# Kernel optimization log

Measured on AMD Instinct MI355X. Metric: run time of the kernel, lower is better.

The kernel has to match this reference:

```python
import jax, jax.numpy as jnp
import numpy as np

B, T, D, H = 2, 2048, 1024, 16
DK = D // H


def setup_inputs() -> dict:
    key = jax.random.key(0)
    ks = jax.random.split(key, 12)
    s = 1.0 / np.sqrt(D)
    inp = {
        "q_inp": jax.random.normal(ks[0], (B, T, D), jnp.float32),
        "k_inp": jax.random.normal(ks[1], (B, T, D), jnp.float32),
        "v_inp": jax.random.normal(ks[2], (B, T, D), jnp.float32),
        # causal mask: True = position is masked out
        "attn_mask": jnp.triu(jnp.ones((T, T), jnp.bool_), k=1),
        "Wq": jax.random.uniform(ks[3], (D, D), jnp.float32, -s, s),
        "bq": jax.random.uniform(ks[4], (D,), jnp.float32, -s, s),
        "Wk": jax.random.uniform(ks[5], (D, D), jnp.float32, -s, s),
        "bk": jax.random.uniform(ks[6], (D,), jnp.float32, -s, s),
        "Wv": jax.random.uniform(ks[7], (D, D), jnp.float32, -s, s),
        "bv": jax.random.uniform(ks[8], (D,), jnp.float32, -s, s),
        "Wo": jax.random.uniform(ks[9], (D, D), jnp.float32, -s, s),
        "bo": jax.random.uniform(ks[10], (D,), jnp.float32, -s, s),
    }
    return inp


def _split_heads(x):
    # [B,T,D] -> [B,H,T,DK]
    Bx, Tx, _ = x.shape
    return x.reshape(Bx, Tx, H, DK).transpose(0, 2, 1, 3)


def reference(q_inp, k_inp, v_inp, attn_mask, Wq, bq, Wk, bk, Wv, bv, Wo, bo):
    Q = _split_heads(q_inp @ Wq + bq)
    K = _split_heads(k_inp @ Wk + bk)
    V = _split_heads(v_inp @ Wv + bv)
    scale = 1.0 / jnp.sqrt(jnp.asarray(DK, Q.dtype))
    scores = jnp.einsum("bhqd,bhkd->bhqk", Q, K) * scale  # [B,H,T,T]
    scores = jnp.where(attn_mask, -jnp.inf, scores)
    attn = jax.nn.softmax(scores, axis=-1)  # dropout p=0 -> identity
    ctx = jnp.einsum("bhqk,bhkd->bhqd", attn, V)
    out = ctx.transpose(0, 2, 1, 3).reshape(B, T, D) @ Wo + bo
    return (out, attn)
```

## Files before the change

### kernel.cpp

```cpp
#include <hip/hip_runtime.h>
#include <hip/hip_bf16.h>
#include <math.h>


typedef unsigned short bfu;
typedef __attribute__((ext_vector_type(8))) short short8;
typedef __attribute__((ext_vector_type(4))) float f32x4;

#define AS1(p) ((const __attribute__((address_space(1))) void*)(p))
#define AS3(p) ((__attribute__((address_space(3))) void*)(p))
#define SOFT_C 16.0f

__device__ __forceinline__ void gld16(const void* g, void* l) {
  __builtin_amdgcn_global_load_lds(AS1(g), AS3(l), 16, 0, 0);
}

__device__ __forceinline__ bfu f2bf(float f) {
  unsigned int u = __float_as_uint(f);
  u = (u + 0x7fffu + ((u >> 16) & 1u)) >> 16;
  return (bfu)u;
}
__device__ __forceinline__ float bf2f(bfu b) {
  return __uint_as_float(((unsigned int)b) << 16);
}
__device__ __forceinline__ short8 lds_read8(const bfu* p) {
  return *reinterpret_cast<const short8*>(p);
}

__global__ __launch_bounds__(256) void cvt_x_kernel(
    const float* __restrict__ q, const float* __restrict__ k,
    const float* __restrict__ v, bfu* __restrict__ out) {
  size_t idx = ((size_t)blockIdx.x * 256 + threadIdx.x) * 8;
  const float* src; size_t off;
  if (idx < 4194304u)       { src = q; off = idx; }
  else if (idx < 8388608u)  { src = k; off = idx - 4194304u; }
  else                      { src = v; off = idx - 8388608u; }
  float4 a = *reinterpret_cast<const float4*>(src + off);
  float4 b = *reinterpret_cast<const float4*>(src + off + 4);
  short8 r;
  r[0] = (short)f2bf(a.x); r[1] = (short)f2bf(a.y);
  r[2] = (short)f2bf(a.z); r[3] = (short)f2bf(a.w);
  r[4] = (short)f2bf(b.x); r[5] = (short)f2bf(b.y);
  r[6] = (short)f2bf(b.z); r[7] = (short)f2bf(b.w);
  *reinterpret_cast<short8*>(out + idx) = r;
}

__global__ __launch_bounds__(256) void cvt_wt_kernel(
    const float* __restrict__ Wq, const float* __restrict__ Wk,
    const float* __restrict__ Wv, const float* __restrict__ Wo,
    bfu* __restrict__ Wt) {
  __shared__ float tile[32][33];
  const int z = blockIdx.z;
  const float* W = z == 0 ? Wq : z == 1 ? Wk : z == 2 ? Wv : Wo;
  bfu* out = Wt + (size_t)z * 1048576;
  const int n0 = blockIdx.x * 32, k0 = blockIdx.y * 32;
  const int tx = threadIdx.x, ty = threadIdx.y;
#pragma unroll
  for (int i = 0; i < 4; ++i)
    tile[ty + i * 8][tx] = W[(size_t)(k0 + ty + i * 8) * 1024 + n0 + tx];
  __syncthreads();
#pragma unroll
  for (int i = 0; i < 4; ++i)
    out[(size_t)(n0 + ty + i * 8) * 1024 + k0 + tx] = f2bf(tile[tx][ty + i * 8]);
}

template <int MODE>
__global__ __launch_bounds__(256) void gemm_bt_kernel(
    const bfu* __restrict__ Aall, const bfu* __restrict__ Btall,
    const float* __restrict__ bias0, const float* __restrict__ bias1,
    const float* __restrict__ bias2, bfu* __restrict__ outQKV,
    float* __restrict__ outF) {
  __shared__ bfu sA[128 * 64];
  __shared__ bfu sB[128 * 64];
  const int z = blockIdx.z;
  const int m0 = blockIdx.x * 128, n0 = blockIdx.y * 128;
  const bfu* A = Aall + (size_t)z * 4194304;
  const bfu* Bt = Btall + (size_t)z * 1048576;
  const float* bias = (z == 0) ? bias0 : (z == 1 ? bias1 : bias2);
  const int tid = threadIdx.x, w = tid >> 6, l = tid & 63;
  const int quad = l >> 4, lane16 = l & 15;
  const int l7 = lane16 & 7;
  const int mb = (w >> 1) * 64, nb = (w & 1) * 64;

  f32x4 acc[4][4] = {};

  for (int kt = 0; kt < 16; ++kt) {
    const int k0 = kt * 64;
    __syncthreads();
#pragma unroll
    for (int j = 0; j < 4; ++j) {
      const int chunk = (w * 4 + j) * 64 + l;
      const int row = chunk >> 3, c = (chunk & 7) ^ (row & 7);
      gld16(A + (size_t)(m0 + row) * 1024 + k0 + c * 8, sA + chunk * 8);
      gld16(Bt + (size_t)(n0 + row) * 1024 + k0 + c * 8, sB + chunk * 8);
    }
    __syncthreads();
#pragma unroll
    for (int ks = 0; ks < 2; ++ks) {
      const int cf = ((ks * 4 + quad) ^ l7) * 8;
      short8 af[4], bfr[4];
#pragma unroll
      for (int x = 0; x < 4; ++x) {
        af[x]  = lds_read8(sA + (mb + x * 16 + lane16) * 64 + cf);
        bfr[x] = lds_read8(sB + (nb + x * 16 + lane16) * 64 + cf);
      }
#pragma unroll
      for (int mi = 0; mi < 4; ++mi)
#pragma unroll
        for (int ni = 0; ni < 4; ++ni)
          acc[mi][ni] = __builtin_amdgcn_mfma_f32_16x16x32_bf16(
              af[mi], bfr[ni], acc[mi][ni], 0, 0, 0);
    }
  }

#pragma unroll
  for (int ni = 0; ni < 4; ++ni) {
    const int n = n0 + nb + ni * 16 + lane16;
    const float bv = bias[n];
#pragma unroll
    for (int mi = 0; mi < 4; ++mi) {
#pragma unroll
      for (int r = 0; r < 4; ++r) {
        const int m = m0 + mb + mi * 16 + quad * 4 + r;
        float v = acc[mi][ni][r] + bv;
        if (MODE == 0) {
          if (z == 0) v *= 0.125f;
          const int b = m >> 11, t = m & 2047;
          const int h = n >> 6, dk = n & 63;
          outQKV[(size_t)z * 4194304 +
                 (((size_t)(b * 16 + h) * 2048 + t) * 64 + dk)] = f2bf(v);
        } else {
          outF[(size_t)m * 1024 + n] = v;
        }
      }
    }
  }
}

__global__ __launch_bounds__(256) void vt_kernel(const bfu* __restrict__ V,
                                                 bfu* __restrict__ vT) {
  __shared__ bfu sT[64][72];
  const int bh = blockIdx.y, t0 = blockIdx.x * 64;
  const int tid = threadIdx.x;
  const bfu* src = V + (size_t)bh * 131072 + (size_t)t0 * 64;
#pragma unroll
  for (int j = 0; j < 2; ++j) {
    const int ch = j * 256 + tid;
    const int row = ch >> 3, c = ch & 7;
    short8 v = *reinterpret_cast<const short8*>(src + row * 64 + c * 8);
#pragma unroll
    for (int e = 0; e < 8; ++e) sT[c * 8 + e][row] = (bfu)v[e];
  }
  __syncthreads();
#pragma unroll
  for (int j = 0; j < 2; ++j) {
    const int ch = j * 256 + tid;
    const int d = ch >> 3, c = ch & 7;
    short8 o = lds_read8(&sT[d][c * 8]);
    *reinterpret_cast<short8*>(vT + (size_t)bh * 131072 + (size_t)d * 2048 +
                               t0 + c * 8) = o;
  }
}

__global__ __launch_bounds__(256) void attn_kernel(
    const bfu* __restrict__ qkv, const bfu* __restrict__ vT,
    float* __restrict__ attnO, bfu* __restrict__ ctx) {
  __shared__ bfu sK[2][64 * 64];
  __shared__ bfu sVt[2][64 * 64];
  __shared__ bfu sP[64 * 72];
  const int linear = (int)blockIdx.y * 16 + (int)blockIdx.x;
  const int bh = (linear & 7) * 4 + (linear >> 7);
  const int x  = (linear >> 3) & 15;
  const int tid = threadIdx.x, w = tid >> 6, l = tid & 63;
  const int quad = l >> 4, lane16 = l & 15;
  const int l7 = lane16 & 7;
  const bfu* Kb = qkv + 4194304 + (size_t)bh * 131072;
  const bfu* VTb = vT + (size_t)bh * 131072;
  const int b = bh >> 4, h = bh & 15;

#pragma unroll 1
  for (int half = 0; half < 2; ++half) {
    const int si = half ? (31 - x) : x;
    const bfu* Qb = qkv + ((size_t)bh * 2048 + si * 64) * 64;
    float* attnRow = attnO + (size_t)bh * 4194304 + (size_t)si * 64 * 2048;

    short8 aq[2];
#pragma unroll
    for (int ks = 0; ks < 2; ++ks)
      aq[ks] = *reinterpret_cast<const short8*>(
          Qb + (size_t)(w * 16 + lane16) * 64 + (ks * 4 + quad) * 8);

    float esum[4] = {};

#pragma unroll
    for (int j = 0; j < 2; ++j) {
      const int chunk = (w * 2 + j) * 64 + l;
      const int row = chunk >> 3, c = (chunk & 7) ^ (row & 7);
      gld16(Kb + row * 64 + c * 8, sK[0] + chunk * 8);
    }
    __syncthreads();
    int cur = 0;
    for (int jj = 0; jj <= si; ++jj) {
      if (jj < si) {
#pragma unroll
        for (int j = 0; j < 2; ++j) {
          const int chunk = (w * 2 + j) * 64 + l;
          const int row = chunk >> 3, c = (chunk & 7) ^ (row & 7);
          gld16(Kb + (size_t)(jj + 1) * 4096 + row * 64 + c * 8,
                sK[cur ^ 1] + chunk * 8);
        }
      }
      f32x4 s[4] = {};
      __builtin_amdgcn_s_setprio(1);
#pragma unroll
      for (int ks = 0; ks < 2; ++ks) {
        const int cf = ((ks * 4 + quad) ^ l7) * 8;
        short8 kb[4];
#pragma unroll
        for (int nf = 0; nf < 4; ++nf)
          kb[nf] = lds_read8(sK[cur] + (nf * 16 + lane16) * 64 + cf);
#pragma unroll
        for (int nf = 0; nf < 4; ++nf)
          s[nf] = __builtin_amdgcn_mfma_f32_16x16x32_bf16(aq[ks], kb[nf],
                                                          s[nf], 0, 0, 0);
      }
      __builtin_amdgcn_s_setprio(0);
      if (jj == si) {
#pragma unroll
        for (int nf = 0; nf < 4; ++nf)
#pragma unroll
          for (int r = 0; r < 4; ++r) {
            const int qg = w * 16 + quad * 4 + r;
            const int kg = nf * 16 + lane16;
            if (kg > qg) s[nf][r] = -INFINITY;
          }
      }
#pragma unroll
      for (int r = 0; r < 4; ++r) {
        float a = __expf(s[0][r] - SOFT_C) + __expf(s[1][r] - SOFT_C);
        float b2 = __expf(s[2][r] - SOFT_C) + __expf(s[3][r] - SOFT_C);
        esum[r] += a + b2;
      }
      __syncthreads();
      cur ^= 1;
    }
    float linv[4];
#pragma unroll
    for (int r = 0; r < 4; ++r) {
      float e = esum[r];
      e += __shfl_xor(e, 1, 64);
      e += __shfl_xor(e, 2, 64);
      e += __shfl_xor(e, 4, 64);
      e += __shfl_xor(e, 8, 64);
      linv[r] = 1.f / e;
    }

    f32x4 o[4] = {};
#pragma unroll
    for (int j = 0; j < 2; ++j) {
      const int chunk = (w * 2 + j) * 64 + l;
      const int row = chunk >> 3, c = (chunk & 7) ^ (row & 7);
      gld16(Kb + row * 64 + c * 8, sK[0] + chunk * 8);
      gld16(VTb + (size_t)row * 2048 + c * 8, sVt[0] + chunk * 8);
    }
    __syncthreads();
    cur = 0;
    for (int jj = 0; jj <= si; ++jj) {
      if (jj < si) {
#pragma unroll
        for (int j = 0; j < 2; ++j) {
          const int chunk = (w * 2 + j) * 64 + l;
          const int row = chunk >> 3, c = (chunk & 7) ^ (row & 7);
          gld16(Kb + (size_t)(jj + 1) * 4096 + row * 64 + c * 8,
                sK[cur ^ 1] + chunk * 8);
          gld16(VTb + (size_t)row * 2048 + (jj + 1) * 64 + c * 8,
                sVt[cur ^ 1] + chunk * 8);
        }
      }
      f32x4 s[4] = {};
      __builtin_amdgcn_s_setprio(1);
#pragma unroll
      for (int ks = 0; ks < 2; ++ks) {
        const int cf = ((ks * 4 + quad) ^ l7) * 8;
        short8 kb[4];
#pragma unroll
        for (int nf = 0; nf < 4; ++nf)
          kb[nf] = lds_read8(sK[cur] + (nf * 16 + lane16) * 64 + cf);
#pragma unroll
        for (int nf = 0; nf < 4; ++nf)
          s[nf] = __builtin_amdgcn_mfma_f32_16x16x32_bf16(aq[ks], kb[nf],
                                                          s[nf], 0, 0, 0);
      }
      __builtin_amdgcn_s_setprio(0);
      if (jj == si) {
#pragma unroll
        for (int nf = 0; nf < 4; ++nf)
#pragma unroll
          for (int r = 0; r < 4; ++r) {
            const int qg = w * 16 + quad * 4 + r;
            const int kg = nf * 16 + lane16;
            if (kg > qg) s[nf][r] = -INFINITY;
          }
      }
#pragma unroll
      for (int nf = 0; nf < 4; ++nf)
#pragma unroll
        for (int r = 0; r < 4; ++r) {
          const float p = __expf(s[nf][r] - SOFT_C) * linv[r];
          sP[(w * 16 + quad * 4 + r) * 72 + nf * 16 + lane16] = f2bf(p);
        }
      __builtin_amdgcn_s_setprio(1);
#pragma unroll
      for (int ks = 0; ks < 2; ++ks) {
        const int cf = ((ks * 4 + quad) ^ l7) * 8;
        short8 ap, vb[4];
        ap = lds_read8(sP + (w * 16 + lane16) * 72 + ks * 32 + quad * 8);
#pragma unroll
        for (int nf = 0; nf < 4; ++nf)
          vb[nf] = lds_read8(sVt[cur] + (nf * 16 + lane16) * 64 + cf);
#pragma unroll
        for (int nf = 0; nf < 4; ++nf)
          o[nf] = __builtin_amdgcn_mfma_f32_16x16x32_bf16(ap, vb[nf], o[nf],
                                                          0, 0, 0);
      }
      __builtin_amdgcn_s_setprio(0);
#pragma unroll
      for (int it = 0; it < 2; ++it) {
        const int lin = it * 64 + l;
        const int row = lin >> 3, ch = (lin & 7) * 8;
        short8 pv = lds_read8(sP + (w * 16 + row) * 72 + ch);
        float4 f0, f1;
        f0.x = bf2f((bfu)pv[0]); f0.y = bf2f((bfu)pv[1]);
        f0.z = bf2f((bfu)pv[2]); f0.w = bf2f((bfu)pv[3]);
        f1.x = bf2f((bfu)pv[4]); f1.y = bf2f((bfu)pv[5]);
        f1.z = bf2f((bfu)pv[6]); f1.w = bf2f((bfu)pv[7]);
        float* gp = attnRow + (size_t)(w * 16 + row) * 2048 + jj * 64 + ch;
        *reinterpret_cast<float4*>(gp) = f0;
        *reinterpret_cast<float4*>(gp + 4) = f1;
      }
      __syncthreads();
      cur ^= 1;
    }

    {
      const int colz = (si + 1) * 64;
      const int nz4 = (2048 - colz) >> 2;
      const float4 z4 = {0.f, 0.f, 0.f, 0.f};
      for (int r = 0; r < 16; ++r) {
        float* rp = attnRow + (size_t)(w * 16 + r) * 2048 + colz;
        for (int c = l; c < nz4; c += 64) reinterpret_cast<float4*>(rp)[c] = z4;
      }
    }

#pragma unroll
    for (int nf = 0; nf < 4; ++nf)
#pragma unroll
      for (int r = 0; r < 4; ++r)
        sP[(w * 16 + quad * 4 + r) * 72 + nf * 16 + lane16] = f2bf(o[nf][r]);
    __syncthreads();
#pragma unroll
    for (int it = 0; it < 2; ++it) {
      const int lin = it * 256 + tid;
      const int row = lin >> 3, ch = (lin & 7) * 8;
      short8 v = lds_read8(sP + row * 72 + ch);
      *reinterpret_cast<short8*>(
          ctx + ((size_t)(b * 2048 + si * 64 + row)) * 1024 + h * 64 + ch) = v;
    }
    __syncthreads();
  }
}

extern "C" void kernel_launch(void* const* d_in, const int* in_sizes, int n_in,
                              void* d_out, int out_size, void* d_ws,
                              size_t ws_size, hipStream_t stream) {
  const float* q_inp = (const float*)d_in[0];
  const float* k_inp = (const float*)d_in[1];
  const float* v_inp = (const float*)d_in[2];
  const float* Wq = (const float*)d_in[4];
  const float* bq = (const float*)d_in[5];
  const float* Wk = (const float*)d_in[6];
  const float* bk = (const float*)d_in[7];
  const float* Wv = (const float*)d_in[8];
  const float* bv = (const float*)d_in[9];
  const float* Wo = (const float*)d_in[10];
  const float* bo = (const float*)d_in[11];

  bfu* X   = (bfu*)d_ws;
  bfu* Wt  = X + 12582912;
  bfu* qkv = Wt + 4194304;
  bfu* ctx = qkv + 12582912;
  bfu* vT  = X;
  float* out  = (float*)d_out;
  float* attn = out + 4194304;

  cvt_x_kernel<<<6144, 256, 0, stream>>>(q_inp, k_inp, v_inp, X);
  cvt_wt_kernel<<<dim3(32, 32, 4), dim3(32, 8), 0, stream>>>(Wq, Wk, Wv, Wo, Wt);
  gemm_bt_kernel<0><<<dim3(32, 8, 3), 256, 0, stream>>>(X, Wt, bq, bk, bv, qkv,
                                                        nullptr);
  vt_kernel<<<dim3(32, 32), 256, 0, stream>>>(qkv + 8388608, vT);
  attn_kernel<<<dim3(16, 32), 256, 0, stream>>>(qkv, vT, attn, ctx);
  gemm_bt_kernel<1><<<dim3(32, 8, 1), 256, 0, stream>>>(ctx, Wt + 3 * 1048576,
                                                        bo, bo, bo, nullptr, out);
}
```

Baseline: 749.2 us.

## Fuse V transpose into QKV GEMM epilogue and merge conversion kernels

The two fp32-to-bf16 conversion kernels become a single prep launch. The separate V-transpose kernel is removed: the QKV GEMM's V slice now stages its output tile through LDS and writes V directly in transposed [bh][dk][t] layout, straight into the buffer the attention kernel reads. This saves two launches and one full read and write of V, at the cost of an extra LDS round trip and barriers in the GEMM epilogue. Launch bounds hint at two blocks per CU.

```diff
diff --git a/kernel.cpp b/kernel.cpp
--- a/kernel.cpp
+++ b/kernel.cpp
@@ -27,51 +27,54 @@
   return *reinterpret_cast<const short8*>(p);
 }
 
-__global__ __launch_bounds__(256) void cvt_x_kernel(
+__global__ __launch_bounds__(256) void prep_kernel(
     const float* __restrict__ q, const float* __restrict__ k,
-    const float* __restrict__ v, bfu* __restrict__ out) {
-  size_t idx = ((size_t)blockIdx.x * 256 + threadIdx.x) * 8;
-  const float* src; size_t off;
-  if (idx < 4194304u)       { src = q; off = idx; }
-  else if (idx < 8388608u)  { src = k; off = idx - 4194304u; }
-  else                      { src = v; off = idx - 8388608u; }
-  float4 a = *reinterpret_cast<const float4*>(src + off);
-  float4 b = *reinterpret_cast<const float4*>(src + off + 4);
-  short8 r;
-  r[0] = (short)f2bf(a.x); r[1] = (short)f2bf(a.y);
-  r[2] = (short)f2bf(a.z); r[3] = (short)f2bf(a.w);
-  r[4] = (short)f2bf(b.x); r[5] = (short)f2bf(b.y);
-  r[6] = (short)f2bf(b.z); r[7] = (short)f2bf(b.w);
-  *reinterpret_cast<short8*>(out + idx) = r;
-}
-
-__global__ __launch_bounds__(256) void cvt_wt_kernel(
-    const float* __restrict__ Wq, const float* __restrict__ Wk,
-    const float* __restrict__ Wv, const float* __restrict__ Wo,
-    bfu* __restrict__ Wt) {
+    const float* __restrict__ v, const float* __restrict__ Wq,
+    const float* __restrict__ Wk, const float* __restrict__ Wv,
+    const float* __restrict__ Wo, bfu* __restrict__ X, bfu* __restrict__ Wt) {
   __shared__ float tile[32][33];
-  const int z = blockIdx.z;
-  const float* W = z == 0 ? Wq : z == 1 ? Wk : z == 2 ? Wv : Wo;
-  bfu* out = Wt + (size_t)z * 1048576;
-  const int n0 = blockIdx.x * 32, k0 = blockIdx.y * 32;
-  const int tx = threadIdx.x, ty = threadIdx.y;
-#pragma unroll
-  for (int i = 0; i < 4; ++i)
-    tile[ty + i * 8][tx] = W[(size_t)(k0 + ty + i * 8) * 1024 + n0 + tx];
-  __syncthreads();
-#pragma unroll
-  for (int i = 0; i < 4; ++i)
-    out[(size_t)(n0 + ty + i * 8) * 1024 + k0 + tx] = f2bf(tile[tx][ty + i * 8]);
+  const int bid = blockIdx.x, tid = threadIdx.x;
+  if (bid < 6144) {
+    size_t idx = ((size_t)bid * 256 + tid) * 8;
+    const float* src; size_t off;
+    if (idx < 4194304u)       { src = q; off = idx; }
+    else if (idx < 8388608u)  { src = k; off = idx - 4194304u; }
+    else                      { src = v; off = idx - 8388608u; }
+    float4 a = *reinterpret_cast<const float4*>(src + off);
+    float4 b = *reinterpret_cast<const float4*>(src + off + 4);
+    short8 r;
+    r[0] = (short)f2bf(a.x); r[1] = (short)f2bf(a.y);
+    r[2] = (short)f2bf(a.z); r[3] = (short)f2bf(a.w);
+    r[4] = (short)f2bf(b.x); r[5] = (short)f2bf(b.y);
+    r[6] = (short)f2bf(b.z); r[7] = (short)f2bf(b.w);
+    *reinterpret_cast<short8*>(X + idx) = r;
+  } else {
+    const int rem = bid - 6144;
+    const int z = rem >> 10, rr = rem & 1023;
+    const int n0 = (rr & 31) * 32, k0 = (rr >> 5) * 32;
+    const float* W = z == 0 ? Wq : z == 1 ? Wk : z == 2 ? Wv : Wo;
+    bfu* out = Wt + (size_t)z * 1048576;
+    const int tx = tid & 31, ty = tid >> 5;
+#pragma unroll
+    for (int i = 0; i < 4; ++i)
+      tile[ty + i * 8][tx] = W[(size_t)(k0 + ty + i * 8) * 1024 + n0 + tx];
+    __syncthreads();
+#pragma unroll
+    for (int i = 0; i < 4; ++i)
+      out[(size_t)(n0 + ty + i * 8) * 1024 + k0 + tx] =
+          f2bf(tile[tx][ty + i * 8]);
+  }
 }
 
 template <int MODE>
-__global__ __launch_bounds__(256) void gemm_bt_kernel(
+__global__ __launch_bounds__(256, 2) void gemm_bt_kernel(
     const bfu* __restrict__ Aall, const bfu* __restrict__ Btall,
     const float* __restrict__ bias0, const float* __restrict__ bias1,
     const float* __restrict__ bias2, bfu* __restrict__ outQKV,
     float* __restrict__ outF) {
-  __shared__ bfu sA[128 * 64];
-  __shared__ bfu sB[128 * 64];
+  __shared__ bfu sAB[2 * 128 * 64];
+  bfu* sA = sAB;
+  bfu* sB = sAB + 128 * 64;
   const int z = blockIdx.z;
   const int m0 = blockIdx.x * 128, n0 = blockIdx.y * 128;
   const bfu* A = Aall + (size_t)z * 4194304;
@@ -111,6 +114,41 @@
           acc[mi][ni] = __builtin_amdgcn_mfma_f32_16x16x32_bf16(
               af[mi], bfr[ni], acc[mi][ni], 0, 0, 0);
     }
+  }
+
+  if (MODE == 0 && z == 2) {
+    __syncthreads();
+#pragma unroll
+    for (int ni = 0; ni < 4; ++ni) {
+      const int n = nb + ni * 16 + lane16;
+      const float bv = bias[n0 + n];
+      const int s = (n & 15) << 3;
+#pragma unroll
+      for (int mi = 0; mi < 4; ++mi) {
+        const int m4 = mb + mi * 16 + quad * 4;
+        short4 pk;
+        pk.x = (short)f2bf(acc[mi][ni][0] + bv);
+        pk.y = (short)f2bf(acc[mi][ni][1] + bv);
+        pk.z = (short)f2bf(acc[mi][ni][2] + bv);
+        pk.w = (short)f2bf(acc[mi][ni][3] + bv);
+        *reinterpret_cast<short4*>(sAB + n * 128 + (m4 ^ s)) = pk;
+      }
+    }
+    __syncthreads();
+    const int bb = m0 >> 11;
+    const int t0 = m0 & 2047;
+#pragma unroll
+    for (int it = 0; it < 8; ++it) {
+      const int chunk = it * 256 + tid;
+      const int nl = chunk >> 4, mc = (chunk & 15) * 8;
+      const int ss = (nl & 15) << 3;
+      short8 vv = lds_read8(sAB + nl * 128 + (mc ^ ss));
+      const int ng = n0 + nl, hh = ng >> 6, dk = ng & 63;
+      *reinterpret_cast<short8*>(outQKV + 8388608 +
+                                 ((size_t)(bb * 16 + hh) * 64 + dk) * 2048 +
+                                 t0 + mc) = vv;
+    }
+    return;
   }
 
 #pragma unroll
@@ -134,31 +172,6 @@
         }
       }
     }
-  }
-}
-
-__global__ __launch_bounds__(256) void vt_kernel(const bfu* __restrict__ V,
-                                                 bfu* __restrict__ vT) {
-  __shared__ bfu sT[64][72];
-  const int bh = blockIdx.y, t0 = blockIdx.x * 64;
-  const int tid = threadIdx.x;
-  const bfu* src = V + (size_t)bh * 131072 + (size_t)t0 * 64;
-#pragma unroll
-  for (int j = 0; j < 2; ++j) {
-    const int ch = j * 256 + tid;
-    const int row = ch >> 3, c = ch & 7;
-    short8 v = *reinterpret_cast<const short8*>(src + row * 64 + c * 8);
-#pragma unroll
-    for (int e = 0; e < 8; ++e) sT[c * 8 + e][row] = (bfu)v[e];
-  }
-  __syncthreads();
-#pragma unroll
-  for (int j = 0; j < 2; ++j) {
-    const int ch = j * 256 + tid;
-    const int d = ch >> 3, c = ch & 7;
-    short8 o = lds_read8(&sT[d][c * 8]);
-    *reinterpret_cast<short8*>(vT + (size_t)bh * 131072 + (size_t)d * 2048 +
-                               t0 + c * 8) = o;
   }
 }
 
@@ -388,16 +401,15 @@
   bfu* X   = (bfu*)d_ws;
   bfu* Wt  = X + 12582912;
   bfu* qkv = Wt + 4194304;
+  bfu* vT  = qkv + 8388608;
   bfu* ctx = qkv + 12582912;
-  bfu* vT  = X;
   float* out  = (float*)d_out;
   float* attn = out + 4194304;
 
-  cvt_x_kernel<<<6144, 256, 0, stream>>>(q_inp, k_inp, v_inp, X);
-  cvt_wt_kernel<<<dim3(32, 32, 4), dim3(32, 8), 0, stream>>>(Wq, Wk, Wv, Wo, Wt);
+  prep_kernel<<<10240, 256, 0, stream>>>(q_inp, k_inp, v_inp, Wq, Wk, Wv, Wo,
+                                         X, Wt);
   gemm_bt_kernel<0><<<dim3(32, 8, 3), 256, 0, stream>>>(X, Wt, bq, bk, bv, qkv,
                                                         nullptr);
-  vt_kernel<<<dim3(32, 32), 256, 0, stream>>>(qkv + 8388608, vT);
   attn_kernel<<<dim3(16, 32), 256, 0, stream>>>(qkv, vT, attn, ctx);
   gemm_bt_kernel<1><<<dim3(32, 8, 1), 256, 0, stream>>>(ctx, Wt + 3 * 1048576,
                                                         bo, bo, bo, nullptr, out);
```

After: 731.4 us. 2.4% less time.
